# Kernel optimization log

Measured on AMD Instinct MI355X. Metric: run time of the kernel, lower is better.

Reference implementation:

```python
import jax, jax.numpy as jnp
import numpy as np

DIM, HEADS, HD = 256, 8, 32
WS, GT, SR = 8, 1, 2
B_, H0, W0 = 4, 128, 128
SCALE = HD ** -0.5


def _bilinear_up_align(x, s):
    # x: (B, C, h, w) -> (B, C, h*s, w*s), bilinear, align_corners=True (matches torch)
    B, C, h, w = x.shape
    oh, ow = h * s, w * s
    def coords(n, o):
        pos = jnp.arange(o, dtype=jnp.float32) * ((n - 1) / (o - 1))
        i0 = jnp.clip(jnp.floor(pos).astype(jnp.int32), 0, n - 2)
        t = pos - i0.astype(jnp.float32)
        return i0, t
    y0, ty = coords(h, oh)
    x0, tx = coords(w, ow)
    top = x[:, :, y0, :] * (1 - ty)[:, None] + x[:, :, y0 + 1, :] * ty[:, None]
    return top[:, :, :, x0] * (1 - tx) + top[:, :, :, x0 + 1] * tx


def _layernorm(x, w, b, eps=1e-5):
    mu = x.mean(-1, keepdims=True)
    var = x.var(-1, keepdims=True)
    return (x - mu) * jax.lax.rsqrt(var + eps) * w + b


def setup_inputs() -> dict:
    key = jax.random.key(0)
    ks = jax.random.split(key, 8)
    w = lambda k, shape: jax.random.normal(k, shape, jnp.float32) * 0.02
    return {
        "x": jax.random.normal(ks[0], (B_, H0 * W0, DIM), jnp.float32),
        "gt": jax.random.normal(ks[1], (B_, H0 // WS, W0 // WS, GT, DIM), jnp.float32),
        "q_w": w(ks[2], (DIM, DIM)), "q_b": jnp.zeros((DIM,), jnp.float32),
        "kv_w": w(ks[3], (2 * DIM, DIM)), "kv_b": jnp.zeros((2 * DIM,), jnp.float32),
        "sr_w": w(ks[4], (DIM, DIM, SR, SR)), "sr_b": jnp.zeros((DIM,), jnp.float32),
        "norm_w": jnp.ones((DIM,), jnp.float32), "norm_b": jnp.zeros((DIM,), jnp.float32),
        "proj_w": w(ks[5], (DIM, DIM)), "proj_b": jnp.zeros((DIM,), jnp.float32),
        "H": H0, "W": W0,
    }


def reference(x, gt, q_w, q_b, kv_w, kv_b, sr_w, sr_b, norm_w, norm_b, proj_w, proj_b, H, W):
    Bb, Np, C = x.shape
    nH, nW = H // WS, W // WS  # H, W multiples of WS -> no padding branch
    xm = x.reshape(Bb, H, W, C)
    # window partition -> (B, WS*WS, C), B = Bb*nH*nW
    xw = xm.reshape(Bb, nH, WS, nW, WS, C).transpose(0, 1, 3, 2, 4, 5).reshape(-1, WS * WS, C)
    g = gt.reshape(-1, GT, C)  # gt grid already matches (nH, nW)
    skip = g
    xc = jnp.concatenate([g, xw], axis=1)  # (B, N, C), N = GT + WS*WS
    B, N, _ = xc.shape
    q = (xc @ q_w.T + q_b).reshape(B, N, HEADS, HD).transpose(0, 2, 1, 3)  # (B,h,N,d)
    # spatial-reduction KV branch (sr_ratio > 1, gt_num != 0)
    x_ = xw.transpose(0, 2, 1).reshape(B, C, WS, WS)
    x_ = _bilinear_up_align(x_, SR)  # (B, C, WS*SR, WS*SR)
    x_ = jax.lax.conv_general_dilated(
        x_, sr_w, (SR, SR), "VALID",
        dimension_numbers=("NCHW", "OIHW", "NCHW")) + sr_b[None, :, None, None]  # (B,C,WS,WS)
    x_ = _layernorm(x_.reshape(B, C, -1).transpose(0, 2, 1), norm_w, norm_b)
    x_ = jnp.concatenate([g, x_], axis=1)  # (B, N, C)
    kv = (x_ @ kv_w.T + kv_b).reshape(B, -1, 2, HEADS, HD).transpose(2, 0, 3, 1, 4)
    k, v = kv[0], kv[1]  # (B,h,N,d)
    attn = jax.nn.softmax(jnp.einsum("bhnd,bhmd->bhnm", q, k) * SCALE, axis=-1)
    out = jnp.einsum("bhnm,bhmd->bhnd", attn, v).transpose(0, 2, 1, 3).reshape(B, N, C)
    out = out @ proj_w.T + proj_b
    gt_out = out[:, :GT, :]
    xo = out[:, GT:, :].reshape(Bb, nH, nW, WS, WS, C)
    xo = xo.transpose(0, 1, 3, 2, 4, 5).reshape(Bb, H, W, C)  # window reverse
    return xo.reshape(Bb, H * W, C), gt_out, skip
```

## Files before the change

### kernel.cpp

```cpp
#include <hip/hip_runtime.h>

typedef __attribute__((ext_vector_type(4))) float f32x4;
typedef __attribute__((ext_vector_type(8))) float f32x8;
typedef __attribute__((ext_vector_type(8))) short bf16x8;
typedef __attribute__((ext_vector_type(2))) uint u32x2;

#define SCALE_ 0.17677669529663687f

__device__ __forceinline__ float bf2f(ushort u){
  union { unsigned i; float f; } v; v.i = ((unsigned)u) << 16; return v.f;
}
__device__ __forceinline__ ushort f2bf(float f){
  union { float f; unsigned i; } v; v.f = f;
  unsigned r = v.i + 0x7fffu + ((v.i >> 16) & 1u);
  return (ushort)(r >> 16);
}
__device__ __forceinline__ void gl16(const void* g, const ushort* l) {
  __builtin_amdgcn_global_load_lds((const __attribute__((address_space(1))) uint*)g,
                                   (__attribute__((address_space(3))) uint*)l, 16, 0, 0);
}

__global__ __launch_bounds__(256) void k_prep(const float* __restrict__ x,
    const float* __restrict__ gt, const float* __restrict__ qw,
    const float* __restrict__ kvw, const float* __restrict__ pw,
    const float* __restrict__ srw, ushort* __restrict__ xc,
    ushort* __restrict__ xkv, float* __restrict__ out2,
    ushort* __restrict__ wq, ushort* __restrict__ wkv,
    ushort* __restrict__ wpr, ushort* __restrict__ wcv)
{
  int blk = blockIdx.x;
  int tid = threadIdx.x;
  if (blk >= 16640) {
    int i = (blk - 16640) * 256 + tid;
    if (i < 65536)            wq[i] = f2bf(qw[i]);
    else if (i < 196608)      wkv[i - 65536] = f2bf(kvw[i - 65536]);
    else if (i < 262144)      wpr[i - 196608] = f2bf(pw[i - 196608]);
    else {
      int j = i - 262144;
      int o = j >> 10, t = (j >> 8) & 3, cc = j & 255;
      wcv[j] = f2bf(srw[o * 1024 + cc * 4 + t]);
    }
    return;
  }
  int row = blk * 4 + (tid >> 6);
  int c4 = (tid & 63) * 4;
  int wi = row / 65, n = row - wi * 65;
  if (n == 0) {
    float4 g4 = *(const float4*)(gt + (size_t)wi * 256 + c4);
    uint lo = (uint)f2bf(g4.x) | ((uint)f2bf(g4.y) << 16);
    uint hi = (uint)f2bf(g4.z) | ((uint)f2bf(g4.w) << 16);
    u32x2 pk = {lo, hi};
    *(u32x2*)(xc  + (size_t)row * 256 + c4) = pk;
    *(u32x2*)(xkv + (size_t)row * 256 + c4) = pk;
    *(float4*)(out2 + (size_t)wi * 256 + c4) = g4;
  } else {
    int s = n - 1, r = s >> 3, cc = s & 7;
    int b = wi >> 8, wh = (wi >> 4) & 15, ww = wi & 15;
    int hw = (wh * 8 + r) * 128 + ww * 8 + cc;
    float4 v4 = *(const float4*)(x + ((size_t)b * 16384 + hw) * 256 + c4);
    uint lo = (uint)f2bf(v4.x) | ((uint)f2bf(v4.y) << 16);
    uint hi = (uint)f2bf(v4.z) | ((uint)f2bf(v4.w) << 16);
    u32x2 pk = {lo, hi};
    *(u32x2*)(xc + (size_t)row * 256 + c4) = pk;
  }
}

template<int N>
__global__ __launch_bounds__(256) void k_gemm2(const ushort* __restrict__ A,
    const ushort* __restrict__ W, const float* __restrict__ bias,
    ushort* __restrict__ C)
{
  constexpr int K = 256;
  __shared__ __align__(16) ushort As[2][128 * 64];
  __shared__ __align__(16) ushort Bs[2][128 * 64];
  int lin = blockIdx.y * gridDim.x + blockIdx.x;
  int qq = (gridDim.x * gridDim.y) >> 3;
  int sw2 = (lin & 7) * qq + (lin >> 3);
  int m0 = (sw2 / gridDim.x) * 128, n0 = (sw2 % gridDim.x) * 128;
  int tid = threadIdx.x, lane = tid & 63;
  int wave = tid >> 6;
  int lm = lane & 15, kg = lane >> 4;
  int wr = wave >> 1, wc = wave & 1;

  const char* Ab = (const char*)A + (size_t)m0 * (K * 2);
  const char* Bb = (const char*)W + (size_t)n0 * (K * 2);

  auto stage = [&](int buf, int kt) {
#pragma unroll
    for (int j = 0; j < 4; ++j) {
      int c = j * 256 + tid;
      int row = c >> 3, slot = c & 7;
      int srcoff = row * (K * 2) + kt * 128 + ((slot * 16) ^ ((row & 7) << 4));
      gl16(Ab + srcoff, (const ushort*)((const char*)As[buf] + c * 16));
      gl16(Bb + srcoff, (const ushort*)((const char*)Bs[buf] + c * 16));
    }
  };

  f32x4 acc[4][4];
  f32x4 zero = {0.f, 0.f, 0.f, 0.f};
#pragma unroll
  for (int a = 0; a < 4; ++a)
#pragma unroll
    for (int b = 0; b < 4; ++b) acc[a][b] = zero;

  stage(0, 0);
  __syncthreads();
#pragma unroll
  for (int t = 0; t < 4; ++t) {
    int cur = t & 1;
    if (t < 3) stage(cur ^ 1, t + 1);
#pragma unroll
    for (int s = 0; s < 2; ++s) {
      int sw = (lm & 7) << 4;
      bf16x8 af[4], bw[4];
#pragma unroll
      for (int mi = 0; mi < 4; ++mi) {
        int row = wr * 64 + mi * 16 + lm;
        af[mi] = *(const bf16x8*)((const char*)As[cur] + row * 128 + ((s * 64 + kg * 16) ^ sw));
      }
#pragma unroll
      for (int ni = 0; ni < 4; ++ni) {
        int row = wc * 64 + ni * 16 + lm;
        bw[ni] = *(const bf16x8*)((const char*)Bs[cur] + row * 128 + ((s * 64 + kg * 16) ^ sw));
      }
#pragma unroll
      for (int mi = 0; mi < 4; ++mi)
#pragma unroll
        for (int ni = 0; ni < 4; ++ni)
          acc[mi][ni] = __builtin_amdgcn_mfma_f32_16x16x32_bf16(af[mi], bw[ni], acc[mi][ni], 0, 0, 0);
    }
    __syncthreads();
  }

  int rbase = m0 + wr * 64 + kg * 4;
#pragma unroll
  for (int ni = 0; ni < 4; ++ni) {
    int col = n0 + wc * 64 + ni * 16 + lm;
    float bv = bias[col];
#pragma unroll
    for (int mi = 0; mi < 4; ++mi) {
#pragma unroll
      for (int r = 0; r < 4; ++r)
        C[(size_t)(rbase + mi * 16 + r) * N + col] = f2bf(acc[mi][ni][r] + bv);
    }
  }
}

__global__ __launch_bounds__(256) void k_gemm_out(const ushort* __restrict__ A,
    const ushort* __restrict__ W, const float* __restrict__ bias,
    float* __restrict__ out)
{
  constexpr int K = 256;
  __shared__ __align__(16) ushort As[2][128 * 64];
  __shared__ __align__(16) ushort Bs[2][128 * 64];
  int lin = blockIdx.y * gridDim.x + blockIdx.x;
  int qq = (gridDim.x * gridDim.y) >> 3;
  int sw2 = (lin & 7) * qq + (lin >> 3);
  int m0 = (sw2 / gridDim.x) * 128, n0 = (sw2 % gridDim.x) * 128;
  int tid = threadIdx.x, lane = tid & 63;
  int wave = tid >> 6;
  int lm = lane & 15, kg = lane >> 4;
  int wr = wave >> 1, wc = wave & 1;

  const char* Ab = (const char*)A + (size_t)m0 * (K * 2);
  const char* Bb = (const char*)W + (size_t)n0 * (K * 2);

  auto stage = [&](int buf, int kt) {
#pragma unroll
    for (int j = 0; j < 4; ++j) {
      int c = j * 256 + tid;
      int row = c >> 3, slot = c & 7;
      int srcoff = row * (K * 2) + kt * 128 + ((slot * 16) ^ ((row & 7) << 4));
      gl16(Ab + srcoff, (const ushort*)((const char*)As[buf] + c * 16));
      gl16(Bb + srcoff, (const ushort*)((const char*)Bs[buf] + c * 16));
    }
  };

  f32x4 acc[4][4];
  f32x4 zero = {0.f, 0.f, 0.f, 0.f};
#pragma unroll
  for (int a = 0; a < 4; ++a)
#pragma unroll
    for (int b = 0; b < 4; ++b) acc[a][b] = zero;

  stage(0, 0);
  __syncthreads();
#pragma unroll
  for (int t = 0; t < 4; ++t) {
    int cur = t & 1;
    if (t < 3) stage(cur ^ 1, t + 1);
#pragma unroll
    for (int s = 0; s < 2; ++s) {
      int sw = (lm & 7) << 4;
      bf16x8 af[4], bw[4];
#pragma unroll
      for (int mi = 0; mi < 4; ++mi) {
        int row = wr * 64 + mi * 16 + lm;
        af[mi] = *(const bf16x8*)((const char*)As[cur] + row * 128 + ((s * 64 + kg * 16) ^ sw));
      }
#pragma unroll
      for (int ni = 0; ni < 4; ++ni) {
        int row = wc * 64 + ni * 16 + lm;
        bw[ni] = *(const bf16x8*)((const char*)Bs[cur] + row * 128 + ((s * 64 + kg * 16) ^ sw));
      }
#pragma unroll
      for (int mi = 0; mi < 4; ++mi)
#pragma unroll
        for (int ni = 0; ni < 4; ++ni)
          acc[mi][ni] = __builtin_amdgcn_mfma_f32_16x16x32_bf16(af[mi], bw[ni], acc[mi][ni], 0, 0, 0);
    }
    __syncthreads();
  }

  int rbase = m0 + wr * 64 + kg * 4;
#pragma unroll
  for (int mi = 0; mi < 4; ++mi) {
#pragma unroll
    for (int r = 0; r < 4; ++r) {
      int g = rbase + mi * 16 + r;
      int wi2 = g / 65;
      int n = g - wi2 * 65;
      size_t dstrow;
      if (n == 0) {
        dstrow = (size_t)(16777216 >> 8) + wi2;
      } else {
        int s = n - 1;
        int b = wi2 >> 8, wh = (wi2 >> 4) & 15, ww = wi2 & 15;
        int r2 = s >> 3, cc = s & 7;
        dstrow = (size_t)(b << 14) + (wh * 8 + r2) * 128 + ww * 8 + cc;
      }
      float* dst = out + dstrow * 256;
#pragma unroll
      for (int ni = 0; ni < 4; ++ni) {
        int col = n0 + wc * 64 + ni * 16 + lm;
        dst[col] = acc[mi][ni][r] + bias[col];
      }
    }
  }
}

__global__ __launch_bounds__(512) void k_conv(const ushort* __restrict__ xc,
    const ushort* __restrict__ wconv, ushort* __restrict__ cconv)
{
  __shared__ ushort U[2][64 * 256];
  int wi = blockIdx.x;
  int tid = threadIdx.x, wave = tid >> 6, lane = tid & 63;
  int lm = lane & 15, kg = lane >> 4;
  const ushort* src = xc + (size_t)(wi * 65 + 1) * 256;
  f32x4 acc[4][2];
  f32x4 zero = {0.f, 0.f, 0.f, 0.f};
#pragma unroll
  for (int a = 0; a < 4; a++)
#pragma unroll
    for (int b = 0; b < 2; b++) acc[a][b] = zero;

  int cb = (tid & 31) * 8;
  int sg = tid >> 5;

  auto build = [&](int t, ushort* Ub) {
    int dy = t >> 1, dx = t & 1;
    for (int s = sg; s < 64; s += 16) {
      int i = s >> 3, j = s & 7;
      int yy = 2 * i + dy, xx = 2 * j + dx;
      float py = yy * (7.0f / 15.0f); int iy = (int)py; if (iy > 6) iy = 6; float ty = py - iy;
      float px = xx * (7.0f / 15.0f); int ix = (int)px; if (ix > 6) ix = 6; float tx = px - ix;
      float w00 = (1.f - ty) * (1.f - tx), w01 = (1.f - ty) * tx;
      float w10 = ty * (1.f - tx), w11 = ty * tx;
      const ushort* p = src + (size_t)(iy * 8 + ix) * 256 + cb;
      bf16x8 p00 = *(const bf16x8*)(p);
      bf16x8 p01 = *(const bf16x8*)(p + 256);
      bf16x8 p10 = *(const bf16x8*)(p + 2048);
      bf16x8 p11 = *(const bf16x8*)(p + 2304);
      bf16x8 o8;
#pragma unroll
      for (int jj = 0; jj < 8; jj++) {
        float v = w00 * bf2f((ushort)p00[jj]) + w01 * bf2f((ushort)p01[jj])
                + w10 * bf2f((ushort)p10[jj]) + w11 * bf2f((ushort)p11[jj]);
        o8[jj] = (short)f2bf(v);
      }
      int byteoff = s * 512 + ((2 * cb) ^ ((s & 7) << 4));
      *(bf16x8*)((char*)Ub + byteoff) = o8;
    }
  };

  build(0, U[0]);
  __syncthreads();
  for (int t = 0; t < 4; t++) {
    const ushort* Ub = U[t & 1];
    const ushort* wc = wconv + t * 256;
    for (int kk = 0; kk < 256; kk += 32) {
      int kb = kk + kg * 8;
      bf16x8 afr[4];
#pragma unroll
      for (int mi = 0; mi < 4; mi++) {
        int srow = mi * 16 + lm;
        int off = (srow * 512 + 2 * kb) ^ ((srow & 7) << 4);
        afr[mi] = *(const bf16x8*)((const char*)Ub + off);
      }
#pragma unroll
      for (int ni = 0; ni < 2; ni++) {
        bf16x8 b = *(const bf16x8*)(wc + (size_t)(wave * 32 + ni * 16 + lm) * 1024 + kb);
#pragma unroll
        for (int mi = 0; mi < 4; mi++)
          acc[mi][ni] = __builtin_amdgcn_mfma_f32_16x16x32_bf16(afr[mi], b, acc[mi][ni], 0, 0, 0);
      }
    }
    if (t < 3) build(t + 1, U[(t + 1) & 1]);
    __syncthreads();
  }

#pragma unroll
  for (int mi = 0; mi < 4; mi++) {
    int row = wi * 64 + mi * 16 + kg * 4;
#pragma unroll
    for (int ni = 0; ni < 2; ni++) {
      int col = wave * 32 + ni * 16 + lm;
#pragma unroll
      for (int r = 0; r < 4; r++)
        cconv[(size_t)(row + r) * 256 + col] = f2bf(acc[mi][ni][r]);
    }
  }
}

__global__ __launch_bounds__(256) void k_ln(const ushort* __restrict__ cconv,
    const float* __restrict__ srb, const float* __restrict__ nw,
    const float* __restrict__ nb, ushort* __restrict__ xkv)
{
  int row = blockIdx.x * 4 + (threadIdx.x >> 6);
  int lane = threadIdx.x & 63;
  const ushort* p = cconv + (size_t)row * 256;
  float v[4]; float sum = 0.f, sq = 0.f;
#pragma unroll
  for (int r = 0; r < 4; r++) {
    int c = r * 64 + lane;
    v[r] = bf2f(p[c]) + srb[c];
    sum += v[r]; sq += v[r] * v[r];
  }
#pragma unroll
  for (int off = 1; off < 64; off <<= 1) {
    sum += __shfl_xor(sum, off, 64);
    sq  += __shfl_xor(sq,  off, 64);
  }
  float mean = sum * (1.f / 256.f);
  float var = sq * (1.f / 256.f) - mean * mean;
  float rs = rsqrtf(var + 1e-5f);
  int wi = row >> 6, s = row & 63;
  ushort* o = xkv + (size_t)(wi * 65 + 1 + s) * 256;
#pragma unroll
  for (int r = 0; r < 4; r++) {
    int c = r * 64 + lane;
    o[c] = f2bf((v[r] - mean) * rs * nw[c] + nb[c]);
  }
}

__global__ __launch_bounds__(256) void k_attn(const ushort* __restrict__ q,
    const ushort* __restrict__ kv, ushort* __restrict__ att)
{
  __shared__ ushort smem[4][8064];
  int wi = blockIdx.x >> 1;
  int tid = threadIdx.x, wave = tid >> 6, lane = tid & 63;
  int h = (blockIdx.x & 1) * 4 + wave;
  int lm = lane & 15, kg = lane >> 4;
  ushort* plds = smem[wave];
  ushort* vt   = smem[wave] + 5760;

  size_t qbase  = (size_t)wi * 65 * 256 + (size_t)h * 32;
  size_t kvbase = (size_t)wi * 65 * 512 + (size_t)h * 32;

  for (int e = lane; e < 2080; e += 64) {
    int m = e >> 5, d = e & 31;
    vt[d * 72 + m] = kv[kvbase + (size_t)m * 512 + 256 + d];
  }

  bf16x8 akf[5], bqf[5];
#pragma unroll
  for (int i = 0; i < 5; i++) {
    akf[i] = *(const bf16x8*)(kv + kvbase + (size_t)(16 * i + lm) * 512 + kg * 8);
    bqf[i] = *(const bf16x8*)(q  + qbase  + (size_t)(16 * i + lm) * 256 + kg * 8);
  }

  f32x4 sc[5][5];
  f32x4 zero = {0.f, 0.f, 0.f, 0.f};
#pragma unroll
  for (int mi = 0; mi < 5; mi++)
#pragma unroll
    for (int nj = 0; nj < 5; nj++) sc[mi][nj] = zero;
#pragma unroll
  for (int mi = 0; mi < 5; mi++)
#pragma unroll
    for (int nj = 0; nj < 5; nj++)
      sc[mi][nj] = __builtin_amdgcn_mfma_f32_16x16x32_bf16(akf[mi], bqf[nj], sc[mi][nj], 0, 0, 0);

  const float C = SCALE_ * 1.4426950408889634f;
  float inv[5], p64b[5];
#pragma unroll
  for (int nj = 0; nj < 5; nj++) {
    float s4 = sc[4][nj][0];
    float mx = (kg == 0) ? s4 : -1e30f;
#pragma unroll
    for (int mi = 0; mi < 4; mi++)
#pragma unroll
      for (int r = 0; r < 4; r++) mx = fmaxf(mx, sc[mi][nj][r]);
    mx = fmaxf(mx, __shfl_xor(mx, 16, 64));
    mx = fmaxf(mx, __shfl_xor(mx, 32, 64));
    float sum = 0.f;
#pragma unroll
    for (int mi = 0; mi < 4; mi++)
#pragma unroll
      for (int r = 0; r < 4; r++) {
        float e = exp2f((sc[mi][nj][r] - mx) * C);
        sc[mi][nj][r] = e; sum += e;
      }
    float e4 = exp2f((s4 - mx) * C);
    sum += (kg == 0) ? e4 : 0.f;
    sum += __shfl_xor(sum, 16, 64);
    sum += __shfl_xor(sum, 32, 64);
    inv[nj] = 1.0f / sum;
    p64b[nj] = __shfl(e4, lm, 64);
  }

#pragma unroll
  for (int nj = 0; nj < 5; nj++) {
    int n = 16 * nj + lm;
#pragma unroll
    for (int mi = 0; mi < 4; mi++) {
      uint lo = (uint)f2bf(sc[mi][nj][0]) | ((uint)f2bf(sc[mi][nj][1]) << 16);
      uint hi = (uint)f2bf(sc[mi][nj][2]) | ((uint)f2bf(sc[mi][nj][3]) << 16);
      u32x2 pk = {lo, hi};
      *(u32x2*)(plds + n * 72 + 16 * mi + 4 * kg) = pk;
    }
  }

  f32x4 od[2][5];
#pragma unroll
  for (int dt = 0; dt < 2; dt++)
#pragma unroll
    for (int nj = 0; nj < 5; nj++) od[dt][nj] = zero;
#pragma unroll
  for (int c = 0; c < 2; c++) {
    bf16x8 av[2], bp[5];
#pragma unroll
    for (int dt = 0; dt < 2; dt++)
      av[dt] = *(const bf16x8*)(vt + (16 * dt + lm) * 72 + c * 32 + kg * 8);
#pragma unroll
    for (int nj = 0; nj < 5; nj++)
      bp[nj] = *(const bf16x8*)(plds + (16 * nj + lm) * 72 + c * 32 + kg * 8);
#pragma unroll
    for (int dt = 0; dt < 2; dt++)
#pragma unroll
      for (int nj = 0; nj < 5; nj++)
        od[dt][nj] = __builtin_amdgcn_mfma_f32_16x16x32_bf16(av[dt], bp[nj], od[dt][nj], 0, 0, 0);
  }
  float v64[8];
#pragma unroll
  for (int dt = 0; dt < 2; dt++)
#pragma unroll
    for (int r = 0; r < 4; r++)
      v64[dt * 4 + r] = bf2f(vt[(16 * dt + 4 * kg + r) * 72 + 64]);
#pragma unroll
  for (int dt = 0; dt < 2; dt++)
#pragma unroll
    for (int nj = 0; nj < 5; nj++)
#pragma unroll
      for (int r = 0; r < 4; r++)
        od[dt][nj][r] += v64[dt * 4 + r] * p64b[nj];

#pragma unroll
  for (int nj = 0; nj < 5; nj++) {
    int n = 16 * nj + lm;
    float scl = inv[nj];
#pragma unroll
    for (int dt = 0; dt < 2; dt++) {
      uint lo = (uint)f2bf(od[dt][nj][0] * scl) | ((uint)f2bf(od[dt][nj][1] * scl) << 16);
      uint hi = (uint)f2bf(od[dt][nj][2] * scl) | ((uint)f2bf(od[dt][nj][3] * scl) << 16);
      u32x2 pk = {lo, hi};
      *(u32x2*)(plds + n * 40 + 16 * dt + 4 * kg) = pk;
    }
  }
  size_t abase = (size_t)wi * 65 * 256 + (size_t)h * 32;
  for (int e = lane; e < 1040; e += 64) {
    int n = e >> 4, d2 = e & 15;
    *(uint*)(att + abase + (size_t)n * 256 + 2 * d2) = *(const uint*)(plds + n * 40 + 2 * d2);
  }
}

extern "C" void kernel_launch(void* const* d_in, const int* in_sizes, int n_in,
                              void* d_out, int out_size, void* d_ws, size_t ws_size,
                              hipStream_t stream)
{
  const float* x    = (const float*)d_in[0];
  const float* gt   = (const float*)d_in[1];
  const float* q_w  = (const float*)d_in[2];
  const float* q_b  = (const float*)d_in[3];
  const float* kv_w = (const float*)d_in[4];
  const float* kv_b = (const float*)d_in[5];
  const float* sr_w = (const float*)d_in[6];
  const float* sr_b = (const float*)d_in[7];
  const float* nw   = (const float*)d_in[8];
  const float* nb   = (const float*)d_in[9];
  const float* p_w  = (const float*)d_in[10];
  const float* p_b  = (const float*)d_in[11];
  (void)in_sizes; (void)n_in; (void)out_size;

  if (ws_size < 204996608u) return;
  char* ws = (char*)d_ws;
  ushort* xc  = (ushort*)(ws);
  ushort* qb  = (ushort*)(ws + 34078720);
  ushort* xkv = (ushort*)(ws + 68157440);
  ushort* kv  = (ushort*)(ws + 102236160);
  ushort* ccv = (ushort*)(ws + 170393600);
  ushort* wq  = (ushort*)(ws + 203948032);
  ushort* wkv = (ushort*)(ws + 204079104);
  ushort* wpr = (ushort*)(ws + 204341248);
  ushort* wcv = (ushort*)(ws + 204472320);

  float* out = (float*)d_out;
  float* out2 = out + 16777216 + 262144;

  k_prep<<<18688, 256, 0, stream>>>(x, gt, q_w, kv_w, p_w, sr_w,
                                    xc, xkv, out2, wq, wkv, wpr, wcv);
  k_gemm2<256><<<dim3(2, 520), 256, 0, stream>>>(xc, wq, q_b, qb);
  k_conv<<<1024, 512, 0, stream>>>(xc, wcv, ccv);
  k_ln<<<16384, 256, 0, stream>>>(ccv, sr_b, nw, nb, xkv);
  k_gemm2<512><<<dim3(4, 520), 256, 0, stream>>>(xkv, wkv, kv_b, kv);
  k_attn<<<2048, 256, 0, stream>>>(qb, kv, xc);
  k_gemm_out<<<dim3(2, 520), 256, 0, stream>>>(xc, wpr, p_b, out);
}
```

Baseline: 240.2 us.

## Fuse LayerNorm into conv kernel and use separable bilinear upsample build

Folds the LayerNorm pass into the end of the conv kernel. The conv result plus bias is staged in shared memory, normalized per row and written straight to the KV input buffer, which removes the intermediate bf16 conv buffer and a separate kernel launch. The upsample build is also made separable: each thread interpolates five rows vertically, then emits four horizontally interpolated outputs with compile-time weights, which cuts the global loads and multiplies per output. The cost is a longer tail inside the conv kernel where only 8 rows are normalized per wave iteration, plus an extra barrier.

```diff
diff --git a/kernel.cpp b/kernel.cpp
--- a/kernel.cpp
+++ b/kernel.cpp
@@ -239,14 +239,79 @@
   }
 }
 
+__device__ __forceinline__ f32x8 row_lerp_g(const ushort* src, int row, int cg, float ty) {
+  const ushort* a0 = src + (size_t)row * 256 + cg * 8;
+  bf16x8 a = *(const bf16x8*)(a0);
+  bf16x8 b = *(const bf16x8*)(a0 + 2048);
+  f32x8 h;
+#pragma unroll
+  for (int e = 0; e < 8; ++e) {
+    float av = bf2f((ushort)a[e]);
+    h[e] = av + ty * (bf2f((ushort)b[e]) - av);
+  }
+  return h;
+}
+__device__ __forceinline__ void emit_u(char* U, const f32x8& Ha, const f32x8& Hb,
+                                       float tx, int s, int cg) {
+  bf16x8 o8;
+#pragma unroll
+  for (int e = 0; e < 8; ++e) {
+    float lv = Ha[e];
+    o8[e] = (short)f2bf(lv + tx * (Hb[e] - lv));
+  }
+  *(bf16x8*)(U + s * 512 + ((cg * 16) ^ ((s & 7) << 4))) = o8;
+}
+
+template<int XH, int DX>
+__device__ __forceinline__ void conv_build(const ushort* src, char* U,
+                                           int dy, int i, int cg)
+{
+  int yy = 2 * i + dy;
+  float py = yy * (7.0f / 15.0f);
+  int iy = (int)py; if (iy > 6) iy = 6;
+  float ty = py - iy;
+  constexpr int j0 = XH * 3;
+  int rb = iy * 8 + j0;
+  f32x8 H0 = row_lerp_g(src, rb + 0, cg, ty);
+  f32x8 H1 = row_lerp_g(src, rb + 1, cg, ty);
+  f32x8 H2 = row_lerp_g(src, rb + 2, cg, ty);
+  f32x8 H3 = row_lerp_g(src, rb + 3, cg, ty);
+  f32x8 H4 = row_lerp_g(src, rb + 4, cg, ty);
+  int sb = i * 8 + XH * 4;
+  if (XH == 0 && DX == 0) {
+    emit_u(U, H0, H1, 0.0f,        sb + 0, cg);
+    emit_u(U, H0, H1, 14.f / 15.f, sb + 1, cg);
+    emit_u(U, H1, H2, 13.f / 15.f, sb + 2, cg);
+    emit_u(U, H2, H3, 12.f / 15.f, sb + 3, cg);
+  } else if (XH == 0 && DX == 1) {
+    emit_u(U, H0, H1,  7.f / 15.f, sb + 0, cg);
+    emit_u(U, H1, H2,  6.f / 15.f, sb + 1, cg);
+    emit_u(U, H2, H3,  5.f / 15.f, sb + 2, cg);
+    emit_u(U, H3, H4,  4.f / 15.f, sb + 3, cg);
+  } else if (XH == 1 && DX == 0) {
+    emit_u(U, H0, H1, 11.f / 15.f, sb + 0, cg);
+    emit_u(U, H1, H2, 10.f / 15.f, sb + 1, cg);
+    emit_u(U, H2, H3,  9.f / 15.f, sb + 2, cg);
+    emit_u(U, H3, H4,  8.f / 15.f, sb + 3, cg);
+  } else {
+    emit_u(U, H1, H2,  3.f / 15.f, sb + 0, cg);
+    emit_u(U, H2, H3,  2.f / 15.f, sb + 1, cg);
+    emit_u(U, H3, H4,  1.f / 15.f, sb + 2, cg);
+    emit_u(U, H3, H4,  1.0f,       sb + 3, cg);
+  }
+}
+
 __global__ __launch_bounds__(512) void k_conv(const ushort* __restrict__ xc,
-    const ushort* __restrict__ wconv, ushort* __restrict__ cconv)
-{
-  __shared__ ushort U[2][64 * 256];
+    const ushort* __restrict__ wconv, const float* __restrict__ srb,
+    const float* __restrict__ nw, const float* __restrict__ nb,
+    ushort* __restrict__ xkv)
+{
+  __shared__ __align__(16) ushort U[2][64 * 256];
   int wi = blockIdx.x;
   int tid = threadIdx.x, wave = tid >> 6, lane = tid & 63;
   int lm = lane & 15, kg = lane >> 4;
   const ushort* src = xc + (size_t)(wi * 65 + 1) * 256;
+
   f32x4 acc[4][2];
   f32x4 zero = {0.f, 0.f, 0.f, 0.f};
 #pragma unroll
@@ -254,38 +319,19 @@
 #pragma unroll
     for (int b = 0; b < 2; b++) acc[a][b] = zero;
 
-  int cb = (tid & 31) * 8;
-  int sg = tid >> 5;
-
-  auto build = [&](int t, ushort* Ub) {
+  int cg = tid & 31;
+  int i = (tid >> 5) & 7;
+  int xh = tid >> 8;
+
+  auto build = [&](int t, char* Ub) {
     int dy = t >> 1, dx = t & 1;
-    for (int s = sg; s < 64; s += 16) {
-      int i = s >> 3, j = s & 7;
-      int yy = 2 * i + dy, xx = 2 * j + dx;
-      float py = yy * (7.0f / 15.0f); int iy = (int)py; if (iy > 6) iy = 6; float ty = py - iy;
-      float px = xx * (7.0f / 15.0f); int ix = (int)px; if (ix > 6) ix = 6; float tx = px - ix;
-      float w00 = (1.f - ty) * (1.f - tx), w01 = (1.f - ty) * tx;
-      float w10 = ty * (1.f - tx), w11 = ty * tx;
-      const ushort* p = src + (size_t)(iy * 8 + ix) * 256 + cb;
-      bf16x8 p00 = *(const bf16x8*)(p);
-      bf16x8 p01 = *(const bf16x8*)(p + 256);
-      bf16x8 p10 = *(const bf16x8*)(p + 2048);
-      bf16x8 p11 = *(const bf16x8*)(p + 2304);
-      bf16x8 o8;
-#pragma unroll
-      for (int jj = 0; jj < 8; jj++) {
-        float v = w00 * bf2f((ushort)p00[jj]) + w01 * bf2f((ushort)p01[jj])
-                + w10 * bf2f((ushort)p10[jj]) + w11 * bf2f((ushort)p11[jj]);
-        o8[jj] = (short)f2bf(v);
-      }
-      int byteoff = s * 512 + ((2 * cb) ^ ((s & 7) << 4));
-      *(bf16x8*)((char*)Ub + byteoff) = o8;
-    }
+    if (dx == 0) { if (xh == 0) conv_build<0, 0>(src, Ub, dy, i, cg);
+                   else         conv_build<1, 0>(src, Ub, dy, i, cg); }
+    else         { if (xh == 0) conv_build<0, 1>(src, Ub, dy, i, cg);
+                   else         conv_build<1, 1>(src, Ub, dy, i, cg); }
   };
 
-  build(0, U[0]);
-  __syncthreads();
-  for (int t = 0; t < 4; t++) {
+  auto mfma_tap = [&](int t) {
     const ushort* Ub = U[t & 1];
     const ushort* wc = wconv + t * 256;
     for (int kk = 0; kk < 256; kk += 32) {
@@ -305,51 +351,58 @@
           acc[mi][ni] = __builtin_amdgcn_mfma_f32_16x16x32_bf16(afr[mi], b, acc[mi][ni], 0, 0, 0);
       }
     }
-    if (t < 3) build(t + 1, U[(t + 1) & 1]);
+  };
+
+  build(0, (char*)U[0]);
+  __syncthreads();
+  for (int t = 0; t < 4; t++) {
+    mfma_tap(t);
+    if (t < 3) build(t + 1, (char*)U[(t + 1) & 1]);
     __syncthreads();
   }
 
-#pragma unroll
-  for (int mi = 0; mi < 4; mi++) {
-    int row = wi * 64 + mi * 16 + kg * 4;
-#pragma unroll
-    for (int ni = 0; ni < 2; ni++) {
-      int col = wave * 32 + ni * 16 + lm;
-#pragma unroll
-      for (int r = 0; r < 4; r++)
-        cconv[(size_t)(row + r) * 256 + col] = f2bf(acc[mi][ni][r]);
-    }
-  }
-}
-
-__global__ __launch_bounds__(256) void k_ln(const ushort* __restrict__ cconv,
-    const float* __restrict__ srb, const float* __restrict__ nw,
-    const float* __restrict__ nb, ushort* __restrict__ xkv)
-{
-  int row = blockIdx.x * 4 + (threadIdx.x >> 6);
-  int lane = threadIdx.x & 63;
-  const ushort* p = cconv + (size_t)row * 256;
-  float v[4]; float sum = 0.f, sq = 0.f;
-#pragma unroll
-  for (int r = 0; r < 4; r++) {
-    int c = r * 64 + lane;
-    v[r] = bf2f(p[c]) + srb[c];
-    sum += v[r]; sq += v[r] * v[r];
-  }
-#pragma unroll
-  for (int off = 1; off < 64; off <<= 1) {
-    sum += __shfl_xor(sum, off, 64);
-    sq  += __shfl_xor(sq,  off, 64);
-  }
-  float mean = sum * (1.f / 256.f);
-  float var = sq * (1.f / 256.f) - mean * mean;
-  float rs = rsqrtf(var + 1e-5f);
-  int wi = row >> 6, s = row & 63;
-  ushort* o = xkv + (size_t)(wi * 65 + 1 + s) * 256;
-#pragma unroll
-  for (int r = 0; r < 4; r++) {
-    int c = r * 64 + lane;
-    o[c] = f2bf((v[r] - mean) * rs * nw[c] + nb[c]);
+  char* P = (char*)U[0];
+  float sb0 = srb[wave * 32 + lm];
+  float sb1 = srb[wave * 32 + 16 + lm];
+#pragma unroll
+  for (int mi = 0; mi < 4; ++mi) {
+#pragma unroll
+    for (int ni = 0; ni < 2; ++ni) {
+#pragma unroll
+      for (int r = 0; r < 4; ++r) {
+        int s = mi * 16 + kg * 4 + r;
+        int c = wave * 32 + ni * 16 + lm;
+        float v = acc[mi][ni][r] + (ni ? sb1 : sb0);
+        *(ushort*)(P + s * 512 + ((2 * c) ^ ((s & 7) << 4))) = f2bf(v);
+      }
+    }
+  }
+  __syncthreads();
+
+  ushort* orow = xkv + (size_t)(wi * 65 + 1) * 256;
+#pragma unroll
+  for (int it = 0; it < 8; ++it) {
+    int row = it * 8 + wave;
+    float v[4]; float sum = 0.f, sq = 0.f;
+#pragma unroll
+    for (int j = 0; j < 4; ++j) {
+      int c = j * 64 + lane;
+      v[j] = bf2f(*(const ushort*)(P + row * 512 + ((2 * c) ^ ((row & 7) << 4))));
+      sum += v[j]; sq += v[j] * v[j];
+    }
+#pragma unroll
+    for (int off = 1; off < 64; off <<= 1) {
+      sum += __shfl_xor(sum, off, 64);
+      sq  += __shfl_xor(sq,  off, 64);
+    }
+    float mean = sum * (1.f / 256.f);
+    float var = sq * (1.f / 256.f) - mean * mean;
+    float rs = rsqrtf(var + 1e-5f);
+#pragma unroll
+    for (int j = 0; j < 4; ++j) {
+      int c = j * 64 + lane;
+      orow[(size_t)row * 256 + c] = f2bf((v[j] - mean) * rs * nw[c] + nb[c]);
+    }
   }
 }
 
@@ -508,7 +561,6 @@
   ushort* qb  = (ushort*)(ws + 34078720);
   ushort* xkv = (ushort*)(ws + 68157440);
   ushort* kv  = (ushort*)(ws + 102236160);
-  ushort* ccv = (ushort*)(ws + 170393600);
   ushort* wq  = (ushort*)(ws + 203948032);
   ushort* wkv = (ushort*)(ws + 204079104);
   ushort* wpr = (ushort*)(ws + 204341248);
@@ -520,8 +572,7 @@
   k_prep<<<18688, 256, 0, stream>>>(x, gt, q_w, kv_w, p_w, sr_w,
                                     xc, xkv, out2, wq, wkv, wpr, wcv);
   k_gemm2<256><<<dim3(2, 520), 256, 0, stream>>>(xc, wq, q_b, qb);
-  k_conv<<<1024, 512, 0, stream>>>(xc, wcv, ccv);
-  k_ln<<<16384, 256, 0, stream>>>(ccv, sr_b, nw, nb, xkv);
+  k_conv<<<1024, 512, 0, stream>>>(xc, wcv, sr_b, nw, nb, xkv);
   k_gemm2<512><<<dim3(4, 520), 256, 0, stream>>>(xkv, wkv, kv_b, kv);
   k_attn<<<2048, 256, 0, stream>>>(qb, kv, xc);
   k_gemm_out<<<dim3(2, 520), 256, 0, stream>>>(xc, wpr, p_b, out);
```

Result: slower. 245.1 us (+2.1%).
